# Performance work log

Hardware: AMD Instinct MI355X
Metric: run time of the kernel (lower is better)

## Reference

```python
import jax, jax.numpy as jnp
import numpy as np

EPS = 1e-08


def setup_inputs() -> dict:
    key = jax.random.key(0)
    k1, k2, k3 = jax.random.split(key, 3)
    n = 8192
    risk = jax.random.normal(k1, (n,), dtype=jnp.float32)
    t = jax.random.uniform(k2, (n,), dtype=jnp.float32)
    e = jax.random.randint(k3, (n,), 0, 2).astype(jnp.float32)
    return {"risk": risk, "t": t, "e": e}


def reference(risk, t, e):
    # R_mat[i, j] = (t[j] >= t[i])  -- risk set for sample i
    theta = risk.reshape(-1)                      # [n]
    exp_theta = jnp.exp(theta)                    # [n]
    R = (t[None, :] >= t[:, None]).astype(theta.dtype)  # [n, n]
    # sum over j of exp_theta[j] * R[i, j]
    log_sum = jnp.log(R @ exp_theta + EPS)        # [n]
    loss_cox = -jnp.mean((theta - log_sum) * e)
    return loss_cox
```

## Files before the change

### kernel.cpp

```cpp
#include <hip/hip_runtime.h>
#include <math.h>

#define N 8192
#define BS 256
#define EPSV 1e-8f

__global__ __launch_bounds__(BS) void cox_partial(const float* __restrict__ risk,
                                                  const float* __restrict__ t,
                                                  const float* __restrict__ e,
                                                  float* __restrict__ blockPartial) {
    __shared__ float sT[N];
    __shared__ float sE[N];

    const int tid = threadIdx.x;

    const float4* t4g = (const float4*)t;
    const float4* r4g = (const float4*)risk;
    float4* sT4 = (float4*)sT;
    float4* sE4 = (float4*)sE;
    #pragma unroll
    for (int s = 0; s < N / 4 / BS; ++s) {
        int f = tid + s * BS;
        float4 tv = t4g[f];
        float4 rv = r4g[f];
        sT4[f] = tv;
        float4 ev;
        ev.x = __expf(rv.x);
        ev.y = __expf(rv.y);
        ev.z = __expf(rv.z);
        ev.w = __expf(rv.w);
        sE4[f] = ev;
    }
    __syncthreads();

    const int lane = tid & 63;
    const int wave = tid >> 6;
    const int i0 = blockIdx.x * 32 + wave * 8;

    float ti[8];
    #pragma unroll
    for (int m = 0; m < 8; ++m) ti[m] = sT[i0 + m];

    float sum[8];
    #pragma unroll
    for (int m = 0; m < 8; ++m) sum[m] = 0.0f;

    #pragma unroll 2
    for (int k = 0; k < N / 4 / 64; ++k) {
        int f = lane + (k << 6);
        float4 tj = sT4[f];
        float4 ej = sE4[f];
        #pragma unroll
        for (int m = 0; m < 8; ++m) {
            float s0 = (tj.x >= ti[m]) ? ej.x : 0.0f;
            float s1 = (tj.y >= ti[m]) ? ej.y : 0.0f;
            float s2 = (tj.z >= ti[m]) ? ej.z : 0.0f;
            float s3 = (tj.w >= ti[m]) ? ej.w : 0.0f;
            sum[m] += (s0 + s1) + (s2 + s3);
        }
    }

    float myS = 0.0f;
    #pragma unroll
    for (int m = 0; m < 8; ++m) {
        float v = sum[m];
        v += __shfl_xor(v, 32);
        v += __shfl_xor(v, 16);
        v += __shfl_xor(v, 8);
        v += __shfl_xor(v, 4);
        v += __shfl_xor(v, 2);
        v += __shfl_xor(v, 1);
        if (lane == m) myS = v;
    }

    float contrib = 0.0f;
    if (lane < 8) {
        int i = i0 + lane;
        contrib = e[i] * (risk[i] - __logf(myS + EPSV));
    }

    __syncthreads();
    if (lane < 8) sT[wave * 8 + lane] = contrib;
    __syncthreads();
    if (tid == 0) {
        float tot = 0.0f;
        #pragma unroll
        for (int x = 0; x < 32; ++x) tot += sT[x];
        blockPartial[blockIdx.x] = tot;
    }
}

__global__ __launch_bounds__(BS) void cox_final(const float* __restrict__ blockPartial,
                                                float* __restrict__ out) {
    const int tid = threadIdx.x;
    float v = blockPartial[tid];
    v += __shfl_xor(v, 32);
    v += __shfl_xor(v, 16);
    v += __shfl_xor(v, 8);
    v += __shfl_xor(v, 4);
    v += __shfl_xor(v, 2);
    v += __shfl_xor(v, 1);
    __shared__ float sW[4];
    if ((tid & 63) == 0) sW[tid >> 6] = v;
    __syncthreads();
    if (tid == 0) {
        float tot = sW[0] + sW[1] + sW[2] + sW[3];
        out[0] = -tot * (1.0f / (float)N);
    }
}

extern "C" void kernel_launch(void* const* d_in, const int* in_sizes, int n_in,
                              void* d_out, int out_size, void* d_ws, size_t ws_size,
                              hipStream_t stream) {
    const float* risk = (const float*)d_in[0];
    const float* t    = (const float*)d_in[1];
    const float* e    = (const float*)d_in[2];
    float* out = (float*)d_out;
    float* part = (float*)d_ws;

    cox_partial<<<N / 32, BS, 0, stream>>>(risk, t, e, part);
    cox_final<<<1, BS, 0, stream>>>(part, out);
}
```

Measured before the change: 68.84 us.

## Split j-dimension into chunks across grid, move log/sum to final kernel

New measurement: 68.02 us. No clear change (-1.2%).

```diff
diff --git a/kernel.cpp b/kernel.cpp
--- a/kernel.cpp
+++ b/kernel.cpp
@@ -3,35 +3,37 @@
 
 #define N 8192
 #define BS 256
+#define NCHUNK 4
+#define CHUNK (N / NCHUNK)
 #define EPSV 1e-8f
 
 __global__ __launch_bounds__(BS) void cox_partial(const float* __restrict__ risk,
                                                   const float* __restrict__ t,
-                                                  const float* __restrict__ e,
-                                                  float* __restrict__ blockPartial) {
-    __shared__ float sT[N];
-    __shared__ float sE[N];
+                                                  float* __restrict__ Spart) {
+    __shared__ float sT[CHUNK];
+    __shared__ float sE[CHUNK];
 
     const int tid = threadIdx.x;
+    const int chunk = blockIdx.y;
 
     const float4* t4g = (const float4*)t;
     const float4* r4g = (const float4*)risk;
     float4* sT4 = (float4*)sT;
     float4* sE4 = (float4*)sE;
     #pragma unroll
-    for (int s = 0; s < N / 4 / BS; ++s) {
-        int f = tid + s * BS;
-        float4 tv = t4g[f];
-        float4 rv = r4g[f];
-        sT4[f] = tv;
+    for (int s = 0; s < CHUNK / 4 / BS; ++s) {
+        int fl = tid + s * BS;
+        int fg = chunk * (CHUNK / 4) + fl;
+        float4 tv = t4g[fg];
+        float4 rv = r4g[fg];
+        sT4[fl] = tv;
         float4 ev;
         ev.x = __expf(rv.x);
         ev.y = __expf(rv.y);
         ev.z = __expf(rv.z);
         ev.w = __expf(rv.w);
-        sE4[f] = ev;
+        sE4[fl] = ev;
     }
-    __syncthreads();
 
     const int lane = tid & 63;
     const int wave = tid >> 6;
@@ -39,14 +41,16 @@
 
     float ti[8];
     #pragma unroll
-    for (int m = 0; m < 8; ++m) ti[m] = sT[i0 + m];
+    for (int m = 0; m < 8; ++m) ti[m] = t[i0 + m];
 
     float sum[8];
     #pragma unroll
     for (int m = 0; m < 8; ++m) sum[m] = 0.0f;
 
-    #pragma unroll 2
-    for (int k = 0; k < N / 4 / 64; ++k) {
+    __syncthreads();
+
+    #pragma unroll
+    for (int k = 0; k < CHUNK / 4 / 64; ++k) {
         int f = lane + (k << 6);
         float4 tj = sT4[f];
         float4 ej = sE4[f];
@@ -73,38 +77,41 @@
         if (lane == m) myS = v;
     }
 
-    float contrib = 0.0f;
     if (lane < 8) {
-        int i = i0 + lane;
-        contrib = e[i] * (risk[i] - __logf(myS + EPSV));
+        Spart[chunk * N + i0 + lane] = myS;
+    }
+}
+
+__global__ __launch_bounds__(1024) void cox_final(const float* __restrict__ Spart,
+                                                  const float* __restrict__ risk,
+                                                  const float* __restrict__ e,
+                                                  float* __restrict__ out) {
+    const int tid = threadIdx.x;
+    const int lane = tid & 63;
+    const int wave = tid >> 6;
+
+    float acc = 0.0f;
+    #pragma unroll
+    for (int r = 0; r < N / 1024; ++r) {
+        int i = tid + r * 1024;
+        float S = Spart[i] + Spart[N + i] + Spart[2 * N + i] + Spart[3 * N + i];
+        acc += e[i] * (risk[i] - __logf(S + EPSV));
     }
 
-    __syncthreads();
-    if (lane < 8) sT[wave * 8 + lane] = contrib;
+    acc += __shfl_xor(acc, 32);
+    acc += __shfl_xor(acc, 16);
+    acc += __shfl_xor(acc, 8);
+    acc += __shfl_xor(acc, 4);
+    acc += __shfl_xor(acc, 2);
+    acc += __shfl_xor(acc, 1);
+
+    __shared__ float sW[16];
+    if (lane == 0) sW[wave] = acc;
     __syncthreads();
     if (tid == 0) {
         float tot = 0.0f;
         #pragma unroll
-        for (int x = 0; x < 32; ++x) tot += sT[x];
-        blockPartial[blockIdx.x] = tot;
-    }
-}
-
-__global__ __launch_bounds__(BS) void cox_final(const float* __restrict__ blockPartial,
-                                                float* __restrict__ out) {
-    const int tid = threadIdx.x;
-    float v = blockPartial[tid];
-    v += __shfl_xor(v, 32);
-    v += __shfl_xor(v, 16);
-    v += __shfl_xor(v, 8);
-    v += __shfl_xor(v, 4);
-    v += __shfl_xor(v, 2);
-    v += __shfl_xor(v, 1);
-    __shared__ float sW[4];
-    if ((tid & 63) == 0) sW[tid >> 6] = v;
-    __syncthreads();
-    if (tid == 0) {
-        float tot = sW[0] + sW[1] + sW[2] + sW[3];
+        for (int x = 0; x < 16; ++x) tot += sW[x];
         out[0] = -tot * (1.0f / (float)N);
     }
 }
@@ -115,9 +122,10 @@
     const float* risk = (const float*)d_in[0];
     const float* t    = (const float*)d_in[1];
     const float* e    = (const float*)d_in[2];
-    float* out = (float*)d_out;
+    float* out  = (float*)d_out;
     float* part = (float*)d_ws;
 
-    cox_partial<<<N / 32, BS, 0, stream>>>(risk, t, e, part);
-    cox_final<<<1, BS, 0, stream>>>(part, out);
+    dim3 grid(N / 32, NCHUNK);
+    cox_partial<<<grid, BS, 0, stream>>>(risk, t, part);
+    cox_final<<<1, 1024, 0, stream>>>(part, risk, e, out);
 }
```

## Fuse final reduction via atomicAdd and halve rows per block for more parallelism

Applied to the files above, without the earlier changes.

Result: no change. 69.17 us (+0.5%).

```diff
diff --git a/kernel.cpp b/kernel.cpp
--- a/kernel.cpp
+++ b/kernel.cpp
@@ -3,14 +3,16 @@
 
 #define N 8192
 #define BS 256
+#define NI 16
 #define EPSV 1e-8f
 
-__global__ __launch_bounds__(BS) void cox_partial(const float* __restrict__ risk,
-                                                  const float* __restrict__ t,
-                                                  const float* __restrict__ e,
-                                                  float* __restrict__ blockPartial) {
+__global__ __launch_bounds__(BS) void cox_fused(const float* __restrict__ risk,
+                                                const float* __restrict__ t,
+                                                const float* __restrict__ e,
+                                                float* __restrict__ out) {
     __shared__ float sT[N];
     __shared__ float sE[N];
+    __shared__ float sRed[NI];
 
     const int tid = threadIdx.x;
 
@@ -31,27 +33,28 @@
         ev.w = __expf(rv.w);
         sE4[f] = ev;
     }
-    __syncthreads();
 
     const int lane = tid & 63;
     const int wave = tid >> 6;
-    const int i0 = blockIdx.x * 32 + wave * 8;
+    const int i0 = blockIdx.x * NI + wave * 4;
 
-    float ti[8];
+    float ti[4];
     #pragma unroll
-    for (int m = 0; m < 8; ++m) ti[m] = sT[i0 + m];
+    for (int m = 0; m < 4; ++m) ti[m] = t[i0 + m];
 
-    float sum[8];
+    float sum[4];
     #pragma unroll
-    for (int m = 0; m < 8; ++m) sum[m] = 0.0f;
+    for (int m = 0; m < 4; ++m) sum[m] = 0.0f;
 
-    #pragma unroll 2
+    __syncthreads();
+
+    #pragma unroll 8
     for (int k = 0; k < N / 4 / 64; ++k) {
         int f = lane + (k << 6);
         float4 tj = sT4[f];
         float4 ej = sE4[f];
         #pragma unroll
-        for (int m = 0; m < 8; ++m) {
+        for (int m = 0; m < 4; ++m) {
             float s0 = (tj.x >= ti[m]) ? ej.x : 0.0f;
             float s1 = (tj.y >= ti[m]) ? ej.y : 0.0f;
             float s2 = (tj.z >= ti[m]) ? ej.z : 0.0f;
@@ -62,7 +65,7 @@
 
     float myS = 0.0f;
     #pragma unroll
-    for (int m = 0; m < 8; ++m) {
+    for (int m = 0; m < 4; ++m) {
         float v = sum[m];
         v += __shfl_xor(v, 32);
         v += __shfl_xor(v, 16);
@@ -74,38 +77,18 @@
     }
 
     float contrib = 0.0f;
-    if (lane < 8) {
+    if (lane < 4) {
         int i = i0 + lane;
         contrib = e[i] * (risk[i] - __logf(myS + EPSV));
     }
 
-    __syncthreads();
-    if (lane < 8) sT[wave * 8 + lane] = contrib;
+    if (lane < 4) sRed[wave * 4 + lane] = contrib;
     __syncthreads();
     if (tid == 0) {
         float tot = 0.0f;
         #pragma unroll
-        for (int x = 0; x < 32; ++x) tot += sT[x];
-        blockPartial[blockIdx.x] = tot;
-    }
-}
-
-__global__ __launch_bounds__(BS) void cox_final(const float* __restrict__ blockPartial,
-                                                float* __restrict__ out) {
-    const int tid = threadIdx.x;
-    float v = blockPartial[tid];
-    v += __shfl_xor(v, 32);
-    v += __shfl_xor(v, 16);
-    v += __shfl_xor(v, 8);
-    v += __shfl_xor(v, 4);
-    v += __shfl_xor(v, 2);
-    v += __shfl_xor(v, 1);
-    __shared__ float sW[4];
-    if ((tid & 63) == 0) sW[tid >> 6] = v;
-    __syncthreads();
-    if (tid == 0) {
-        float tot = sW[0] + sW[1] + sW[2] + sW[3];
-        out[0] = -tot * (1.0f / (float)N);
+        for (int x = 0; x < NI; ++x) tot += sRed[x];
+        atomicAdd(out, -tot * (1.0f / (float)N));
     }
 }
 
@@ -116,8 +99,8 @@
     const float* t    = (const float*)d_in[1];
     const float* e    = (const float*)d_in[2];
     float* out = (float*)d_out;
-    float* part = (float*)d_ws;
 
-    cox_partial<<<N / 32, BS, 0, stream>>>(risk, t, e, part);
-    cox_final<<<1, BS, 0, stream>>>(part, out);
+    hipMemsetAsync(out, 0, sizeof(float), stream);
+
+    cox_fused<<<N / NI, BS, 0, stream>>>(risk, t, e, out);
 }
```
